# Performance work log

Measured on AMD Instinct MI355X. Metric: run time of the kernel, lower is better.

Reference implementation:

```python
import jax, jax.numpy as jnp
import numpy as np

KH, KW, PAD, G = 3, 3, 1, 4  # kernel, padding, deformable groups


def _bilinear_gather(xg, py, px):
    """xg: [B,G,C,Hin,Win]; py,px: [B,G,K,H,W] sample coords.
    Returns [B,G,C,K,H,W] with zero padding outside the image (mmcv semantics)."""
    B, Gd, C, Hin, Win = xg.shape
    y0 = jnp.floor(py)
    x0 = jnp.floor(px)
    wy1 = py - y0
    wx1 = px - x0
    wy0 = 1.0 - wy1
    wx0 = 1.0 - wx1
    xf = xg.reshape(B, Gd, C, Hin * Win)

    def gather(yi, xi):
        valid = (yi >= 0) & (yi < Hin) & (xi >= 0) & (xi < Win)
        yc = jnp.clip(yi, 0, Hin - 1).astype(jnp.int32)
        xc = jnp.clip(xi, 0, Win - 1).astype(jnp.int32)
        lin = (yc * Win + xc).reshape(B, Gd, 1, -1)  # [B,G,1,K*H*W]
        v = jnp.take_along_axis(xf, lin, axis=3).reshape(B, Gd, C, *yi.shape[2:])
        return v * valid[:, :, None].astype(xg.dtype)

    return (gather(y0, x0) * (wy0 * wx0)[:, :, None]
            + gather(y0, x0 + 1) * (wy0 * wx1)[:, :, None]
            + gather(y0 + 1, x0) * (wy1 * wx0)[:, :, None]
            + gather(y0 + 1, x0 + 1) * (wy1 * wx1)[:, :, None])


def setup_inputs() -> dict:
    key = jax.random.key(0)
    k1, k2, k3, k4 = jax.random.split(key, 4)
    B, Cin, Cout, H, W = 8, 256, 256, 64, 64
    x = jax.random.normal(k1, (B, Cin, H, W), dtype=jnp.float32)
    shape = jax.random.normal(k2, (B, 4, H, W), dtype=jnp.float32)
    # conv_offset: 1x1 conv, 4 -> G*2*KH*KW = 72 channels, no bias
    w_offset = jax.random.normal(k3, (G * 2 * KH * KW, 4), dtype=jnp.float32) * 0.1
    # conv_adaption: deform conv weight, no bias
    w_deform = jax.random.normal(k4, (Cout, Cin, KH, KW), dtype=jnp.float32) * 0.01
    return {"x": x, "shape": shape, "w_offset": w_offset, "w_deform": w_deform}


def reference(x, shape, w_offset, w_deform):
    B, Cin, H, W = x.shape
    Cout = w_deform.shape[0]
    K = KH * KW
    # 1x1 offset-predicting conv on detached shape
    shape = jax.lax.stop_gradient(shape)
    offset = jnp.einsum('oc,bchw->bohw', w_offset, shape)  # [B, G*2*K, H, W]
    off = offset.reshape(B, G, K, 2, H, W)  # mmcv layout: (dy, dx) per tap
    dy, dx = off[:, :, :, 0], off[:, :, :, 1]  # [B,G,K,H,W]
    # base sampling grid for each kernel tap
    ky, kx = jnp.meshgrid(jnp.arange(KH), jnp.arange(KW), indexing='ij')
    ky = ky.reshape(-1)
    kx = kx.reshape(-1)
    base_y = (ky - PAD)[:, None, None] + jnp.arange(H)[None, :, None]  # [K,H,1]
    base_x = (kx - PAD)[:, None, None] + jnp.arange(W)[None, None, :]  # [K,1,W]
    py = base_y[None, None].astype(x.dtype) + dy  # [B,G,K,H,W]
    px = base_x[None, None].astype(x.dtype) + dx
    xg = x.reshape(B, G, Cin // G, H, W)
    sampled = _bilinear_gather(xg, py, px)  # [B,G,Cpg,K,H,W]
    wr = w_deform.reshape(Cout, G, Cin // G, K)
    out = jnp.einsum('ogck,bgckhw->bohw', wr, sampled)
    return jax.nn.relu(out)
```

## Files before the change

### kernel.cpp

```cpp
#include <hip/hip_runtime.h>
#include <hip/hip_bf16.h>


#define Bn   8
#define CIN  256
#define COUT 256
#define Hn   64
#define Wn   64
#define Gn   4
#define Kn   9
#define CPG  64
#define GK   36

typedef float    f32x4 __attribute__((ext_vector_type(4)));
typedef _Float16 f16x2 __attribute__((ext_vector_type(2)));
typedef _Float16 f16x8 __attribute__((ext_vector_type(8)));

#define SWPAD 1156
#define HWT   32
__global__ void fa_prep(const float* __restrict__ x, const float* __restrict__ w,
                        _Float16* __restrict__ xt, _Float16* __restrict__ wfrag) {
    const int bid = blockIdx.x, t = threadIdx.x;
    __shared__ __align__(16) _Float16 spool[16 * SWPAD];
    if (bid < 1024) {
        _Float16* sT = spool;
        const int b = bid >> 7, tile = bid & 127;
        const int hw0 = tile * HWT;
        const int s = t >> 3, hwq = t & 7;
#pragma unroll
        for (int it = 0; it < 8; it++) {
            int c = it * 32 + s;
            float4 v = *(const float4*)(x + (((size_t)(b * CIN + c)) << 12) + hw0 + hwq * 4);
            const float* vf = (const float*)&v;
#pragma unroll
            for (int j = 0; j < 4; j++) {
                int hw = hwq * 4 + j;
                sT[hw * 256 + (c ^ (hwq << 3))] = (_Float16)vf[j];
            }
        }
        __syncthreads();
        const int cg = t & 31, hwr = t >> 5;
#pragma unroll
        for (int it = 0; it < 4; it++) {
            int hw = it * 8 + hwr;
            int q = hw >> 2;
            f16x8 v = *(const f16x8*)&sT[hw * 256 + ((cg ^ q) << 3)];
            *(f16x8*)&xt[(((size_t)b << 12) + hw0 + hw) * 256 + cg * 8] = v;
        }
    } else {
        _Float16* sw = spool;
        const int mt = (bid - 1024) >> 1, gh = (bid - 1024) & 1;
        const int o0 = mt * 16, g0 = gh * 2;
        const int r = t >> 4, tr = t & 15;
        const float* wp = w + (size_t)(o0 + r) * (CIN * Kn) + g0 * (CPG * Kn);
#pragma unroll
        for (int it = 0; it < 18; it++) {
            int off = it * 64 + tr * 4;
            float4 v = *(const float4*)(wp + off);
            _Float16* d = &sw[r * SWPAD + off];
            d[0] = (_Float16)v.x; d[1] = (_Float16)v.y;
            d[2] = (_Float16)v.z; d[3] = (_Float16)v.w;
        }
        __syncthreads();
#pragma unroll
        for (int it = 0; it < 9; it++) {
            int chunk = it * 256 + t;
            int lane = chunk & 63, ks = (chunk >> 6) & 1, gkl = chunk >> 7;
            int gl = gkl / Kn, k = gkl - gl * Kn;
            int gk = g0 * Kn + gkl;
            int ol = lane & 15;
            int cbase = ks * 32 + (lane >> 4) * 8;
            f16x8 v;
#pragma unroll
            for (int j = 0; j < 8; j++)
                v[j] = sw[ol * SWPAD + (gl * CPG + cbase + j) * Kn + k];
            *(f16x8*)&wfrag[(((size_t)gk * 16 + mt) * 2 + ks) * 512 + lane * 8] = v;
        }
    }
}

__global__ __launch_bounds__(512, 6)
void fa_main(const _Float16* __restrict__ xt, const float* __restrict__ shp,
             const float* __restrict__ w_off, const _Float16* __restrict__ wfrag,
             float* __restrict__ out) {
    const int blk = blockIdx.x;
    const int bp = blk >> 7, h = (blk >> 1) & 63, wh = blk & 1;
    const int w0 = wh * 32;
    const int t = threadIdx.x;
    const int wid = t >> 6, lane = t & 63;
    const int col = lane & 15, quad = lane >> 4;
    const int cg = t & 7, nl = (t >> 3) & 63;

    __shared__ int  s_meta_a[GK * 64];
    __shared__ __align__(8) int2 s_meta_w[GK * 64];
    __shared__ __align__(16) _Float16 sB[2][64 * 64];
    __shared__ float s_shp[2 * 4 * 32];
    __shared__ float s_woff[GK * 8];

    if (t < 256) {
        int bb = t >> 7, c = (t >> 5) & 3, wl = t & 31;
        s_shp[t] = shp[(((bp * 2 + bb) * 4 + c) << 12) + h * Wn + w0 + wl];
    }
    for (int u = t; u < GK * 8; u += 512) s_woff[u] = w_off[u];
    __syncthreads();

    for (int i = t; i < GK * 64; i += 512) {
        int gk = i >> 6, n = i & 63;
        int bb = n >> 5, wl = n & 31;
        int g = gk / Kn, k = gk - g * Kn;
        int ky = k / 3, kx = k - ky * 3;
        float dy = 0.f, dx = 0.f;
#pragma unroll
        for (int c = 0; c < 4; c++) {
            float sv = s_shp[(bb * 4 + c) * 32 + wl];
            dy = fmaf(s_woff[gk * 8 + c],     sv, dy);
            dx = fmaf(s_woff[gk * 8 + 4 + c], sv, dx);
        }
        float py = (float)(h + ky - 1) + dy;
        float px = (float)(w0 + wl + kx - 1) + dx;
        float y0 = floorf(py), x0 = floorf(px);
        float fy = py - y0, fx = px - x0;
        int iy = (int)y0, ix = (int)x0;
        bool y0v = (unsigned)iy       < (unsigned)Hn;
        bool y1v = (unsigned)(iy + 1) < (unsigned)Hn;
        bool x0v = (unsigned)ix       < (unsigned)Wn;
        bool x1v = (unsigned)(ix + 1) < (unsigned)Wn;
        int yc0 = min(max(iy, 0), Hn - 1), yc1 = min(max(iy + 1, 0), Hn - 1);
        int xc0 = min(max(ix, 0), Wn - 1), xc1 = min(max(ix + 1, 0), Wn - 1);
        int l00 = yc0 * Wn + xc0;
        int dx1 = xc1 - xc0, dy1 = yc1 - yc0;
        float wy1 = fy, wy0 = 1.f - fy, wx1 = fx, wx0 = 1.f - fx;
        float w00 = (y0v && x0v) ? wy0 * wx0 : 0.f;
        float w01 = (y0v && x1v) ? wy0 * wx1 : 0.f;
        float w10 = (y1v && x0v) ? wy1 * wx0 : 0.f;
        float w11 = (y1v && x1v) ? wy1 * wx1 : 0.f;
        f16x2 p0, p1;
        p0.x = (_Float16)w00; p0.y = (_Float16)w01;
        p1.x = (_Float16)w10; p1.y = (_Float16)w11;
        s_meta_a[i] = l00 | (dx1 << 12) | (dy1 << 13);
        s_meta_w[i] = make_int2(__builtin_bit_cast(int, p0),
                                __builtin_bit_cast(int, p1));
    }

    f16x8 c4[4];
    int2  amv;
    const unsigned nBase = ((unsigned)(bp * 2 + (nl >> 5)) << 20) + (unsigned)cg * 8u;

    auto issue = [&](int gk) {
        int aw = s_meta_a[gk * 64 + nl];
        amv = s_meta_w[gk * 64 + nl];
        unsigned g = (unsigned)gk / (unsigned)Kn;
        const _Float16* p = xt + nBase + g * 64u;
        unsigned a00 = ((unsigned)aw & 0xFFFu) << 8;
        unsigned dxo = ((unsigned)aw & 0x1000u) >> 4;
        unsigned dyo = ((unsigned)aw & 0x2000u) << 1;
        c4[0] = *(const f16x8*)(p + a00);
        c4[1] = *(const f16x8*)(p + a00 + dxo);
        c4[2] = *(const f16x8*)(p + a00 + dyo);
        c4[3] = *(const f16x8*)(p + a00 + (dxo + dyo));
    };
    auto commit = [&](int buf) {
        f16x2 wv0 = __builtin_bit_cast(f16x2, amv.x);
        f16x2 wv1 = __builtin_bit_cast(f16x2, amv.y);
        f16x2 w00 = __builtin_shufflevector(wv0, wv0, 0, 0);
        f16x2 w01 = __builtin_shufflevector(wv0, wv0, 1, 1);
        f16x2 w10 = __builtin_shufflevector(wv1, wv1, 0, 0);
        f16x2 w11 = __builtin_shufflevector(wv1, wv1, 1, 1);
        const f16x2* a0p = (const f16x2*)&c4[0];
        const f16x2* a1p = (const f16x2*)&c4[1];
        const f16x2* a2p = (const f16x2*)&c4[2];
        const f16x2* a3p = (const f16x2*)&c4[3];
        f16x8 r;
        f16x2* rp = (f16x2*)&r;
#pragma unroll
        for (int p = 0; p < 4; p++) {
            f16x2 rv = w00 * a0p[p] + w01 * a1p[p]
                     + w10 * a2p[p] + w11 * a3p[p];
            rp[p] = rv;
        }
        *(f16x8*)&sB[buf][(nl * 8 + (cg ^ (nl & 7))) * 8] = r;
    };

    f32x4 acc[2][4];
#pragma unroll
    for (int mt = 0; mt < 2; mt++)
#pragma unroll
        for (int nt = 0; nt < 4; nt++) acc[mt][nt] = (f32x4){0.f, 0.f, 0.f, 0.f};

    __syncthreads();

    issue(0);
    commit(0);
    issue(1);
    __syncthreads();

    for (int gk = 0; gk < GK; gk++) {
        const int buf = gk & 1;
        const _Float16* wbase = wfrag + (((size_t)gk * 16 + wid * 2) * 2) * 512;
        f16x8 af[2][2];
#pragma unroll
        for (int ks = 0; ks < 2; ks++)
#pragma unroll
            for (int mt = 0; mt < 2; mt++)
                af[ks][mt] = *(const f16x8*)(wbase + ((size_t)(mt * 2 + ks) * 64 + lane) * 8);
        f16x8 bfv[2][4];
#pragma unroll
        for (int ks = 0; ks < 2; ks++)
#pragma unroll
            for (int nt = 0; nt < 4; nt++) {
                int n = nt * 16 + col;
                int cq8 = ks * 4 + quad;
                bfv[ks][nt] = *(const f16x8*)&sB[buf][(n * 8 + (cq8 ^ (n & 7))) * 8];
            }
        if (gk + 1 < GK) commit(buf ^ 1);
        if (gk + 2 < GK) issue(gk + 2);
#pragma unroll
        for (int ks = 0; ks < 2; ks++)
#pragma unroll
            for (int mt = 0; mt < 2; mt++)
#pragma unroll
                for (int nt = 0; nt < 4; nt++)
                    acc[mt][nt] = __builtin_amdgcn_mfma_f32_16x16x32_f16(
                        af[ks][mt], bfv[ks][nt], acc[mt][nt], 0, 0, 0);
        __syncthreads();
    }

#pragma unroll
    for (int mt = 0; mt < 2; mt++)
#pragma unroll
        for (int r = 0; r < 4; r++) {
            int o = wid * 32 + mt * 16 + quad * 4 + r;
#pragma unroll
            for (int nt = 0; nt < 4; nt++) {
                int n = nt * 16 + col;
                int b = bp * 2 + (n >> 5);
                int w = w0 + (n & 31);
                out[(((size_t)(b * COUT + o)) << 12) + h * Wn + w] =
                    fmaxf(acc[mt][nt][r], 0.f);
            }
        }
}

extern "C" void kernel_launch(void* const* d_in, const int* in_sizes, int n_in,
                              void* d_out, int out_size, void* d_ws, size_t ws_size,
                              hipStream_t stream) {
    const float* x     = (const float*)d_in[0];
    const float* shp   = (const float*)d_in[1];
    const float* w_off = (const float*)d_in[2];
    const float* w_def = (const float*)d_in[3];
    float* out = (float*)d_out;
    _Float16* wfrag = (_Float16*)d_ws;
    _Float16* xt    = (_Float16*)((char*)d_ws + (2u << 20));

    fa_prep<<<1024 + 32, 256, 0, stream>>>(x, w_def, xt, wfrag);
    fa_main<<<512, 512, 0, stream>>>(xt, shp, w_off, wfrag, out);
}
```

Before: 171.2 us.

## Deepen gather/MFMA pipeline with four LDS buffers and half the barriers

Expands the shared-memory B staging from two to four buffers and keeps two register sets of in-flight bilinear gathers. Each gather is issued three steps ahead and committed two steps ahead, so the block barrier runs only once every two k-steps. MFMA sections are wrapped in raised wave priority, and the launch bound is relaxed from 6 to 4 waves per SIMD. The cost is more LDS and more registers per block, which may lower occupancy.

```diff
diff --git a/kernel.cpp b/kernel.cpp
--- a/kernel.cpp
+++ b/kernel.cpp
@@ -79,7 +79,7 @@
     }
 }
 
-__global__ __launch_bounds__(512, 6)
+__global__ __launch_bounds__(512, 4)
 void fa_main(const _Float16* __restrict__ xt, const float* __restrict__ shp,
              const float* __restrict__ w_off, const _Float16* __restrict__ wfrag,
              float* __restrict__ out) {
@@ -93,7 +93,7 @@
 
     __shared__ int  s_meta_a[GK * 64];
     __shared__ __align__(8) int2 s_meta_w[GK * 64];
-    __shared__ __align__(16) _Float16 sB[2][64 * 64];
+    __shared__ __align__(16) _Float16 sB[4][64 * 64];
     __shared__ float s_shp[2 * 4 * 32];
     __shared__ float s_woff[GK * 8];
 
@@ -142,11 +142,11 @@
                                 __builtin_bit_cast(int, p1));
     }
 
-    f16x8 c4[4];
-    int2  amv;
+    f16x8 c4A[4], c4B[4];
+    int2  amvA, amvB;
     const unsigned nBase = ((unsigned)(bp * 2 + (nl >> 5)) << 20) + (unsigned)cg * 8u;
 
-    auto issue = [&](int gk) {
+    auto issue = [&](int gk, f16x8 (&c4)[4], int2& amv) {
         int aw = s_meta_a[gk * 64 + nl];
         amv = s_meta_w[gk * 64 + nl];
         unsigned g = (unsigned)gk / (unsigned)Kn;
@@ -159,7 +159,7 @@
         c4[2] = *(const f16x8*)(p + a00 + dyo);
         c4[3] = *(const f16x8*)(p + a00 + (dxo + dyo));
     };
-    auto commit = [&](int buf) {
+    auto commit = [&](int buf, f16x8 (&c4)[4], int2& amv) {
         f16x2 wv0 = __builtin_bit_cast(f16x2, amv.x);
         f16x2 wv1 = __builtin_bit_cast(f16x2, amv.y);
         f16x2 w00 = __builtin_shufflevector(wv0, wv0, 0, 0);
@@ -189,40 +189,80 @@
 
     __syncthreads();
 
-    issue(0);
-    commit(0);
-    issue(1);
+    issue(0, c4A, amvA);
+    issue(1, c4B, amvB);
+    commit(0, c4A, amvA);
+    issue(2, c4A, amvA);
+    commit(1, c4B, amvB);
     __syncthreads();
 
-    for (int gk = 0; gk < GK; gk++) {
-        const int buf = gk & 1;
-        const _Float16* wbase = wfrag + (((size_t)gk * 16 + wid * 2) * 2) * 512;
-        f16x8 af[2][2];
-#pragma unroll
-        for (int ks = 0; ks < 2; ks++)
-#pragma unroll
-            for (int mt = 0; mt < 2; mt++)
-                af[ks][mt] = *(const f16x8*)(wbase + ((size_t)(mt * 2 + ks) * 64 + lane) * 8);
-        f16x8 bfv[2][4];
-#pragma unroll
-        for (int ks = 0; ks < 2; ks++)
-#pragma unroll
-            for (int nt = 0; nt < 4; nt++) {
-                int n = nt * 16 + col;
-                int cq8 = ks * 4 + quad;
-                bfv[ks][nt] = *(const f16x8*)&sB[buf][(n * 8 + (cq8 ^ (n & 7))) * 8];
-            }
-        if (gk + 1 < GK) commit(buf ^ 1);
-        if (gk + 2 < GK) issue(gk + 2);
-#pragma unroll
-        for (int ks = 0; ks < 2; ks++)
-#pragma unroll
-            for (int mt = 0; mt < 2; mt++)
-#pragma unroll
-                for (int nt = 0; nt < 4; nt++)
-                    acc[mt][nt] = __builtin_amdgcn_mfma_f32_16x16x32_f16(
-                        af[ks][mt], bfv[ks][nt], acc[mt][nt], 0, 0, 0);
-        __syncthreads();
+    for (int jj = 0; jj < GK; jj += 2) {
+        {
+            const int j = jj;
+            const _Float16* wbase = wfrag + (((size_t)j * 16 + wid * 2) * 2) * 512;
+            f16x8 af[2][2];
+#pragma unroll
+            for (int ks = 0; ks < 2; ks++)
+#pragma unroll
+                for (int mt = 0; mt < 2; mt++)
+                    af[ks][mt] = *(const f16x8*)(wbase + ((size_t)(mt * 2 + ks) * 64 + lane) * 8);
+            const _Float16* sBj = sB[j & 3];
+            f16x8 bfv[2][4];
+#pragma unroll
+            for (int ks = 0; ks < 2; ks++)
+#pragma unroll
+                for (int nt = 0; nt < 4; nt++) {
+                    int n = nt * 16 + col;
+                    int cq8 = ks * 4 + quad;
+                    bfv[ks][nt] = *(const f16x8*)&sBj[(n * 8 + (cq8 ^ (n & 7))) * 8];
+                }
+            if (j + 2 < GK) commit((j + 2) & 3, c4A, amvA);
+            if (j + 3 < GK) issue(j + 3, c4B, amvB);
+            __builtin_amdgcn_s_setprio(1);
+#pragma unroll
+            for (int ks = 0; ks < 2; ks++)
+#pragma unroll
+                for (int mt = 0; mt < 2; mt++)
+#pragma unroll
+                    for (int nt = 0; nt < 4; nt++)
+                        acc[mt][nt] = __builtin_amdgcn_mfma_f32_16x16x32_f16(
+                            af[ks][mt], bfv[ks][nt], acc[mt][nt], 0, 0, 0);
+            __builtin_amdgcn_s_setprio(0);
+        }
+        {
+            const int j = jj + 1;
+            const _Float16* wbase = wfrag + (((size_t)j * 16 + wid * 2) * 2) * 512;
+            f16x8 af[2][2];
+#pragma unroll
+            for (int ks = 0; ks < 2; ks++)
+#pragma unroll
+                for (int mt = 0; mt < 2; mt++)
+                    af[ks][mt] = *(const f16x8*)(wbase + ((size_t)(mt * 2 + ks) * 64 + lane) * 8);
+            const _Float16* sBj = sB[j & 3];
+            f16x8 bfv[2][4];
+#pragma unroll
+            for (int ks = 0; ks < 2; ks++)
+#pragma unroll
+                for (int nt = 0; nt < 4; nt++) {
+                    int n = nt * 16 + col;
+                    int cq8 = ks * 4 + quad;
+                    bfv[ks][nt] = *(const f16x8*)&sBj[(n * 8 + (cq8 ^ (n & 7))) * 8];
+                }
+            if (j + 2 < GK) commit((j + 2) & 3, c4B, amvB);
+            if (j + 3 < GK) issue(j + 3, c4A, amvA);
+            __builtin_amdgcn_s_setprio(1);
+#pragma unroll
+            for (int ks = 0; ks < 2; ks++)
+#pragma unroll
+                for (int mt = 0; mt < 2; mt++)
+#pragma unroll
+                    for (int nt = 0; nt < 4; nt++)
+                        acc[mt][nt] = __builtin_amdgcn_mfma_f32_16x16x32_f16(
+                            af[ks][mt], bfv[ks][nt], acc[mt][nt], 0, 0, 0);
+            __builtin_amdgcn_s_setprio(0);
+            asm volatile("s_waitcnt lgkmcnt(0)" ::: "memory");
+            __builtin_amdgcn_s_barrier();
+        }
     }
 
 #pragma unroll
```

New measurement: 172.5 us. Within noise of the previous version (+0.8%).
